# Kernel tuning notes

Hardware: AMD Instinct MI355X
Metric: run time of the kernel (lower is better)

## Reference

```python
import jax, jax.numpy as jnp
import numpy as np

INPUT_DIM = 768
HIDDEN = 64
NUM_CLASSES = 1


def _uniform(key, shape, bound):
    return jax.random.uniform(key, shape, jnp.float32, -bound, bound)


def setup_inputs() -> dict:
    key = jax.random.key(0)
    ks = jax.random.split(key, 16)
    B, T = 128, 512
    bound = 1.0 / np.sqrt(HIDDEN)  # PyTorch RNN init range
    inp = {
        "x": jax.random.normal(ks[0], (B, T, INPUT_DIM), jnp.float32),
        "fixation_num": 1,
        # layer 0: input_dim -> hidden
        "W_ih0": _uniform(ks[1], (HIDDEN, INPUT_DIM), bound),
        "W_hh0": _uniform(ks[2], (HIDDEN, HIDDEN), bound),
        "b_ih0": _uniform(ks[3], (HIDDEN,), bound),
        "b_hh0": _uniform(ks[4], (HIDDEN,), bound),
        # layer 1
        "W_ih1": _uniform(ks[5], (HIDDEN, HIDDEN), bound),
        "W_hh1": _uniform(ks[6], (HIDDEN, HIDDEN), bound),
        "b_ih1": _uniform(ks[7], (HIDDEN,), bound),
        "b_hh1": _uniform(ks[8], (HIDDEN,), bound),
        # layer 2
        "W_ih2": _uniform(ks[9], (HIDDEN, HIDDEN), bound),
        "W_hh2": _uniform(ks[10], (HIDDEN, HIDDEN), bound),
        "b_ih2": _uniform(ks[11], (HIDDEN,), bound),
        "b_hh2": _uniform(ks[12], (HIDDEN,), bound),
        # final linear head
        "fc_w": _uniform(ks[13], (NUM_CLASSES, HIDDEN), bound),
        "fc_b": _uniform(ks[14], (NUM_CLASSES,), bound),
    }
    return inp


def _rnn_layer(x, W_ih, W_hh, b_ih, b_hh):
    # x: [B, T, In] -> hidden sequence [B, T, H]; vanilla tanh RNN, h0 = 0
    pre = jnp.einsum("bti,hi->bth", x, W_ih) + b_ih + b_hh  # input projection for all t
    B = x.shape[0]
    h0 = jnp.zeros((B, W_hh.shape[0]), x.dtype)

    def step(h, p_t):  # p_t: [B, H]
        h = jnp.tanh(p_t + h @ W_hh.T)
        return h, h

    _, hs = jax.lax.scan(step, h0, jnp.swapaxes(pre, 0, 1))  # hs: [T, B, H]
    return jnp.swapaxes(hs, 0, 1)


def reference(x, fixation_num, W_ih0, W_hh0, b_ih0, b_hh0,
              W_ih1, W_hh1, b_ih1, b_hh1,
              W_ih2, W_hh2, b_ih2, b_hh2, fc_w, fc_b):
    # fixation_num is unused by the original forward
    h = _rnn_layer(x, W_ih0, W_hh0, b_ih0, b_hh0)
    h = _rnn_layer(h, W_ih1, W_hh1, b_ih1, b_hh1)
    h = _rnn_layer(h, W_ih2, W_hh2, b_ih2, b_hh2)
    last = h[:, -1, :]  # [B, H]
    return last @ fc_w.T + fc_b  # [B, num_classes]
```

## Files before the change

### kernel.cpp

```cpp
#include <hip/hip_runtime.h>


typedef __fp16 h2_t __attribute__((ext_vector_type(2)));
typedef __fp16 h8_t __attribute__((ext_vector_type(8)));
typedef float  f4_t __attribute__((ext_vector_type(4)));

union F4H { float4 f; h2_t h[4]; };
union H8U { h2_t h2[4]; h8_t h8; };

__device__ __forceinline__ float fdot2(h2_t a, h2_t b, float c) {
    return __builtin_amdgcn_fdot2(a, b, c, false);
}
__device__ __forceinline__ h2_t pack_h2(float x, float y) {
    return __builtin_amdgcn_cvt_pkrtz(x, y);
}
__device__ __forceinline__ float tanh_fast(float x) {
    float e = __expf(2.0f * x);
    return 1.0f - 2.0f * __builtin_amdgcn_rcpf(e + 1.0f);
}

__global__ __launch_bounds__(256) void gemm_pre0(
    const float* __restrict__ x,
    const float* __restrict__ Wih,
    const float* __restrict__ bih, const float* __restrict__ bhh,
    float* __restrict__ pre0)
{
    const int tid = threadIdx.x;
    const int wv  = tid >> 6;
    const int l   = tid & 63;
    const int m   = l & 15;
    const int q   = l >> 4;
    const int rowB = blockIdx.x * 128 + wv * 32;

    const float* ax0 = x + (size_t)(rowB + m) * 768 + q * 8;
    const float* ax1 = x + (size_t)(rowB + 16 + m) * 768 + q * 8;

    float4 ar[2][2];
    float4 br[4][2];

    ar[0][0] = *(const float4*)ax0;       ar[0][1] = *(const float4*)(ax0 + 4);
    ar[1][0] = *(const float4*)ax1;       ar[1][1] = *(const float4*)(ax1 + 4);
#pragma unroll
    for (int nt = 0; nt < 4; ++nt) {
        const float* p = Wih + (size_t)(nt * 16 + m) * 768 + q * 8;
        br[nt][0] = *(const float4*)p;    br[nt][1] = *(const float4*)(p + 4);
    }

    f4_t acc[2][4];
#pragma unroll
    for (int mt = 0; mt < 2; ++mt)
#pragma unroll
        for (int nt = 0; nt < 4; ++nt)
#pragma unroll
            for (int i = 0; i < 4; ++i) acc[mt][nt][i] = 0.0f;

#pragma unroll
    for (int it = 0; it < 24; ++it) {
        H8U fa[2], fb[4];
#pragma unroll
        for (int mt = 0; mt < 2; ++mt) {
            fa[mt].h2[0] = pack_h2(ar[mt][0].x, ar[mt][0].y);
            fa[mt].h2[1] = pack_h2(ar[mt][0].z, ar[mt][0].w);
            fa[mt].h2[2] = pack_h2(ar[mt][1].x, ar[mt][1].y);
            fa[mt].h2[3] = pack_h2(ar[mt][1].z, ar[mt][1].w);
        }
#pragma unroll
        for (int nt = 0; nt < 4; ++nt) {
            fb[nt].h2[0] = pack_h2(br[nt][0].x, br[nt][0].y);
            fb[nt].h2[1] = pack_h2(br[nt][0].z, br[nt][0].w);
            fb[nt].h2[2] = pack_h2(br[nt][1].x, br[nt][1].y);
            fb[nt].h2[3] = pack_h2(br[nt][1].z, br[nt][1].w);
        }
        if (it + 1 < 24) {
            const int ko = (it + 1) * 32;
            ar[0][0] = *(const float4*)(ax0 + ko);
            ar[0][1] = *(const float4*)(ax0 + ko + 4);
            ar[1][0] = *(const float4*)(ax1 + ko);
            ar[1][1] = *(const float4*)(ax1 + ko + 4);
#pragma unroll
            for (int nt = 0; nt < 4; ++nt) {
                const float* p = Wih + (size_t)(nt * 16 + m) * 768 + q * 8 + ko;
                br[nt][0] = *(const float4*)p;
                br[nt][1] = *(const float4*)(p + 4);
            }
        }
#pragma unroll
        for (int mt = 0; mt < 2; ++mt)
#pragma unroll
            for (int nt = 0; nt < 4; ++nt)
                acc[mt][nt] = __builtin_amdgcn_mfma_f32_16x16x32_f16(
                    fa[mt].h8, fb[nt].h8, acc[mt][nt], 0, 0, 0);
    }

    float bn[4];
#pragma unroll
    for (int nt = 0; nt < 4; ++nt) bn[nt] = bih[nt * 16 + m] + bhh[nt * 16 + m];
#pragma unroll
    for (int mt = 0; mt < 2; ++mt)
#pragma unroll
        for (int i = 0; i < 4; ++i) {
            int row = rowB + mt * 16 + q * 4 + i;
            float* pr = pre0 + (size_t)row * 64 + m;
#pragma unroll
            for (int nt = 0; nt < 4; ++nt)
                pr[nt * 16] = acc[mt][nt][i] + bn[nt];
        }
}

__device__ __forceinline__ float layer_epoch(
    const __fp16* __restrict__ in0,
    __fp16* __restrict__ self0, int par,
    const h2_t* wA2, const h2_t* wB2, float bias, int j)
{
    __fp16*       selfPar  = self0 + par * 512;
    const __fp16* selfPrev = self0 + (par ^ 1) * 512;

    F4H u0[8], u1[8];
#pragma unroll
    for (int qq = 0; qq < 8; ++qq) u0[qq].f = *(const float4*)(in0 + qq * 8);

    float hN = 0.0f;
#pragma unroll
    for (int s = 0; s < 8; ++s) {
        const F4H* uc = (s & 1) ? u1 : u0;
        F4H*       un = (s & 1) ? u0 : u1;

        const __fp16* rc = (s == 0) ? (selfPrev + 7 * 64) : (selfPar + (s - 1) * 64);
        F4H uh[8];
#pragma unroll
        for (int qq = 0; qq < 8; ++qq) uh[qq].f = *(const float4*)(rc + qq * 8);

        if (s < 7) {
#pragma unroll
            for (int qq = 0; qq < 8; ++qq)
                un[qq].f = *(const float4*)(in0 + (s + 1) * 64 + qq * 8);
        }

        float x0 = 0.f, x1 = 0.f, x2 = 0.f, x3 = 0.f;
#pragma unroll
        for (int qq = 0; qq < 8; ++qq) {
            x0 = fdot2(wA2[qq * 4 + 0], uc[qq].h[0], x0);
            x1 = fdot2(wA2[qq * 4 + 1], uc[qq].h[1], x1);
            x2 = fdot2(wA2[qq * 4 + 2], uc[qq].h[2], x2);
            x3 = fdot2(wA2[qq * 4 + 3], uc[qq].h[3], x3);
        }
        float xs = (x0 + x1) + (x2 + x3) + bias;

        float a0 = 0.f, a1 = 0.f, a2 = 0.f, a3 = 0.f;
#pragma unroll
        for (int qq = 0; qq < 8; ++qq) {
            a0 = fdot2(wB2[qq * 4 + 0], uh[qq].h[0], a0);
            a1 = fdot2(wB2[qq * 4 + 1], uh[qq].h[1], a1);
            a2 = fdot2(wB2[qq * 4 + 2], uh[qq].h[2], a2);
            a3 = fdot2(wB2[qq * 4 + 3], uh[qq].h[3], a3);
        }
        hN = tanh_fast((a0 + a1) + (a2 + a3) + xs);
        selfPar[s * 64 + j] = (__fp16)hN;
    }
    return hN;
}

__global__ __launch_bounds__(192, 1) void rnn_fused(
    const float* __restrict__ pre0,
    const float* __restrict__ Whh0,
    const float* __restrict__ Wih1, const float* __restrict__ Whh1,
    const float* __restrict__ bih1, const float* __restrict__ bhh1,
    const float* __restrict__ Wih2, const float* __restrict__ Whh2,
    const float* __restrict__ bih2, const float* __restrict__ bhh2,
    const float* __restrict__ fcw, const float* __restrict__ fcb,
    float* __restrict__ out)
{
    const int tid = threadIdx.x;
    const int g   = tid >> 6;
    const int j   = tid & 63;
    const int b   = blockIdx.x;

    __shared__ __align__(16) __fp16 hb[3][2][8][64];

    const float* WA = (g == 0) ? Whh0 : ((g == 1) ? Wih1 : Wih2);
    const float* WB = (g == 0) ? Whh0 : ((g == 1) ? Whh1 : Whh2);
    h2_t wA2[32], wB2[32];
#pragma unroll
    for (int i = 0; i < 32; ++i) {
        wA2[i] = pack_h2(WA[j * 64 + 2 * i], WA[j * 64 + 2 * i + 1]);
        wB2[i] = pack_h2(WB[j * 64 + 2 * i], WB[j * 64 + 2 * i + 1]);
    }
    const float bias = (g == 0) ? 0.0f
                     : ((g == 1) ? (bih1[j] + bhh1[j]) : (bih2[j] + bhh2[j]));

#pragma unroll
    for (int i = 0; i < 8; ++i) ((unsigned int*)hb)[tid + 192 * i] = 0u;

    const size_t pbase = (size_t)b * 32768;
    float pc[8], pn[8];
    if (g == 0) {
#pragma unroll
        for (int s = 0; s < 8; ++s) pc[s] = pre0[pbase + s * 64 + j];
    }
    __syncthreads();

    float hLast = 0.0f;

    for (int e = 0; e < 66; ++e) {
        if (g == 0) {
            if (e < 64) {
                if (e < 63) {
#pragma unroll
                    for (int s = 0; s < 8; ++s)
                        pn[s] = pre0[pbase + (size_t)(e + 1) * 512 + s * 64 + j];
                }
                const int par = e & 1;
#pragma unroll
                for (int s = 0; s < 8; ++s) {
                    const __fp16* rc = (s == 0) ? hb[0][par ^ 1][7] : hb[0][par][s - 1];
                    float a0 = 0.f, a1 = 0.f, a2 = 0.f, a3 = 0.f;
#pragma unroll
                    for (int qq = 0; qq < 8; ++qq) {
                        F4H u; u.f = *(const float4*)&rc[qq * 8];
                        a0 = fdot2(wA2[qq * 4 + 0], u.h[0], a0);
                        a1 = fdot2(wA2[qq * 4 + 1], u.h[1], a1);
                        a2 = fdot2(wA2[qq * 4 + 2], u.h[2], a2);
                        a3 = fdot2(wA2[qq * 4 + 3], u.h[3], a3);
                    }
                    float hN = tanh_fast((a0 + a1) + (a2 + a3) + pc[s]);
                    hb[0][par][s][j] = (__fp16)hN;
                }
#pragma unroll
                for (int s = 0; s < 8; ++s) pc[s] = pn[s];
            }
        } else if (g == 1) {
            if (e >= 1 && e < 65) {
                const int par = (e - 1) & 1;
                layer_epoch(&hb[0][par][0][0], &hb[1][0][0][0], par,
                            wA2, wB2, bias, j);
            }
        } else {
            if (e >= 2) {
                const int par = e & 1;
                float hN = layer_epoch(&hb[1][par][0][0], &hb[2][0][0][0], par,
                                       wA2, wB2, bias, j);
                if (e == 65) hLast = hN;
            }
        }
        __syncthreads();
    }

    if (g == 2) {
        float v = hLast * fcw[j];
#pragma unroll
        for (int m = 1; m < 64; m <<= 1) v += __shfl_xor(v, m, 64);
        if (j == 0) out[b] = v + fcb[0];
    }
}

extern "C" void kernel_launch(void* const* d_in, const int* in_sizes, int n_in,
                              void* d_out, int out_size, void* d_ws, size_t ws_size,
                              hipStream_t stream) {
    const float* x    = (const float*)d_in[0];
    const float* Wih0 = (const float*)d_in[2];
    const float* Whh0 = (const float*)d_in[3];
    const float* bih0 = (const float*)d_in[4];
    const float* bhh0 = (const float*)d_in[5];
    const float* Wih1 = (const float*)d_in[6];
    const float* Whh1 = (const float*)d_in[7];
    const float* bih1 = (const float*)d_in[8];
    const float* bhh1 = (const float*)d_in[9];
    const float* Wih2 = (const float*)d_in[10];
    const float* Whh2 = (const float*)d_in[11];
    const float* bih2 = (const float*)d_in[12];
    const float* bhh2 = (const float*)d_in[13];
    const float* fcw  = (const float*)d_in[14];
    const float* fcb  = (const float*)d_in[15];
    float* out  = (float*)d_out;
    float* pre0 = (float*)d_ws;

    gemm_pre0<<<512, 256, 0, stream>>>(x, Wih0, bih0, bhh0, pre0);
    rnn_fused<<<128, 192, 0, stream>>>(pre0, Whh0, Wih1, Whh1, bih1, bhh1,
                                       Wih2, Whh2, bih2, bhh2, fcw, fcb, out);
}
```

Before: 463.0 us.

## Batch layer 1/2 input projections per epoch with MFMA into shared memory

For layers 1 and 2, the input-to-hidden projection for all 8 timesteps of an epoch is now computed up front with 16x16x32 f16 MFMA instructions. The results go to a shared-memory buffer, replacing the per-timestep fdot2 chain. The serial recurrent loop then only does the hidden-to-hidden dot product plus a shared-memory read, which shortens the per-step critical path of the two slower wave groups. The cost is extra LDS traffic and an MFMA tile that reads 16 rows where only 8 are valid; the extra rows are discarded. Correctness also relies on in-wave ordering of LDS writes and reads without a barrier.

```diff
diff --git a/kernel.cpp b/kernel.cpp
--- a/kernel.cpp
+++ b/kernel.cpp
@@ -5,8 +5,9 @@
 typedef __fp16 h8_t __attribute__((ext_vector_type(8)));
 typedef float  f4_t __attribute__((ext_vector_type(4)));
 
-union F4H { float4 f; h2_t h[4]; };
-union H8U { h2_t h2[4]; h8_t h8; };
+union F4H  { float4 f; h2_t h[4]; };
+union F4H8 { float4 f; h8_t h8; h2_t h2[4]; };
+union H8U  { h2_t h2[4]; h8_t h8; };
 
 __device__ __forceinline__ float fdot2(h2_t a, h2_t b, float c) {
     return __builtin_amdgcn_fdot2(a, b, c, false);
@@ -110,41 +111,45 @@
 __device__ __forceinline__ float layer_epoch(
     const __fp16* __restrict__ in0,
     __fp16* __restrict__ self0, int par,
-    const h2_t* wA2, const h2_t* wB2, float bias, int j)
+    const h2_t* wB2, const h8_t* wX, float* __restrict__ xb,
+    float bias, int j)
 {
     __fp16*       selfPar  = self0 + par * 512;
     const __fp16* selfPrev = self0 + (par ^ 1) * 512;
-
-    F4H u0[8], u1[8];
-#pragma unroll
-    for (int qq = 0; qq < 8; ++qq) u0[qq].f = *(const float4*)(in0 + qq * 8);
+    const int mm = j & 15;
+    const int q4 = j >> 4;
+
+    F4H8 A0, A1;
+    const __fp16* arow = in0 + mm * 64 + q4 * 8;
+    A0.f = *(const float4*)arow;
+    A1.f = *(const float4*)(arow + 32);
+
+    f4_t xacc[4];
+#pragma unroll
+    for (int nt = 0; nt < 4; ++nt) {
+#pragma unroll
+        for (int i = 0; i < 4; ++i) xacc[nt][i] = 0.0f;
+        xacc[nt] = __builtin_amdgcn_mfma_f32_16x16x32_f16(
+            A0.h8, wX[nt * 2 + 0], xacc[nt], 0, 0, 0);
+        xacc[nt] = __builtin_amdgcn_mfma_f32_16x16x32_f16(
+            A1.h8, wX[nt * 2 + 1], xacc[nt], 0, 0, 0);
+    }
+    if (j < 32) {
+#pragma unroll
+        for (int nt = 0; nt < 4; ++nt)
+#pragma unroll
+            for (int i = 0; i < 4; ++i)
+                xb[(q4 * 4 + i) * 64 + nt * 16 + mm] = xacc[nt][i];
+    }
 
     float hN = 0.0f;
 #pragma unroll
     for (int s = 0; s < 8; ++s) {
-        const F4H* uc = (s & 1) ? u1 : u0;
-        F4H*       un = (s & 1) ? u0 : u1;
-
         const __fp16* rc = (s == 0) ? (selfPrev + 7 * 64) : (selfPar + (s - 1) * 64);
         F4H uh[8];
 #pragma unroll
         for (int qq = 0; qq < 8; ++qq) uh[qq].f = *(const float4*)(rc + qq * 8);
-
-        if (s < 7) {
-#pragma unroll
-            for (int qq = 0; qq < 8; ++qq)
-                un[qq].f = *(const float4*)(in0 + (s + 1) * 64 + qq * 8);
-        }
-
-        float x0 = 0.f, x1 = 0.f, x2 = 0.f, x3 = 0.f;
-#pragma unroll
-        for (int qq = 0; qq < 8; ++qq) {
-            x0 = fdot2(wA2[qq * 4 + 0], uc[qq].h[0], x0);
-            x1 = fdot2(wA2[qq * 4 + 1], uc[qq].h[1], x1);
-            x2 = fdot2(wA2[qq * 4 + 2], uc[qq].h[2], x2);
-            x3 = fdot2(wA2[qq * 4 + 3], uc[qq].h[3], x3);
-        }
-        float xs = (x0 + x1) + (x2 + x3) + bias;
+        float xs = xb[s * 64 + j];
 
         float a0 = 0.f, a1 = 0.f, a2 = 0.f, a3 = 0.f;
 #pragma unroll
@@ -154,7 +159,7 @@
             a2 = fdot2(wB2[qq * 4 + 2], uh[qq].h[2], a2);
             a3 = fdot2(wB2[qq * 4 + 3], uh[qq].h[3], a3);
         }
-        hN = tanh_fast((a0 + a1) + (a2 + a3) + xs);
+        hN = tanh_fast((a0 + a1) + (a2 + a3) + xs + bias);
         selfPar[s * 64 + j] = (__fp16)hN;
     }
     return hN;
@@ -176,15 +181,30 @@
     const int b   = blockIdx.x;
 
     __shared__ __align__(16) __fp16 hb[3][2][8][64];
-
-    const float* WA = (g == 0) ? Whh0 : ((g == 1) ? Wih1 : Wih2);
+    __shared__ __align__(16) float  xb2[2][8][64];
+
     const float* WB = (g == 0) ? Whh0 : ((g == 1) ? Whh1 : Whh2);
-    h2_t wA2[32], wB2[32];
-#pragma unroll
-    for (int i = 0; i < 32; ++i) {
-        wA2[i] = pack_h2(WA[j * 64 + 2 * i], WA[j * 64 + 2 * i + 1]);
+    h2_t wB2[32];
+#pragma unroll
+    for (int i = 0; i < 32; ++i)
         wB2[i] = pack_h2(WB[j * 64 + 2 * i], WB[j * 64 + 2 * i + 1]);
-    }
+
+    const float* WX = (g == 1) ? Wih1 : ((g == 2) ? Wih2 : Whh0);
+    const int mm = j & 15, q4 = j >> 4;
+    h8_t wX[8];
+#pragma unroll
+    for (int nt = 0; nt < 4; ++nt)
+#pragma unroll
+        for (int c = 0; c < 2; ++c) {
+            const float* p = WX + (nt * 16 + mm) * 64 + c * 32 + q4 * 8;
+            float4 r0 = *(const float4*)p;
+            float4 r1 = *(const float4*)(p + 4);
+            H8U u;
+            u.h2[0] = pack_h2(r0.x, r0.y); u.h2[1] = pack_h2(r0.z, r0.w);
+            u.h2[2] = pack_h2(r1.x, r1.y); u.h2[3] = pack_h2(r1.z, r1.w);
+            wX[nt * 2 + c] = u.h8;
+        }
+
     const float bias = (g == 0) ? 0.0f
                      : ((g == 1) ? (bih1[j] + bhh1[j]) : (bih2[j] + bhh2[j]));
 
@@ -217,10 +237,10 @@
 #pragma unroll
                     for (int qq = 0; qq < 8; ++qq) {
                         F4H u; u.f = *(const float4*)&rc[qq * 8];
-                        a0 = fdot2(wA2[qq * 4 + 0], u.h[0], a0);
-                        a1 = fdot2(wA2[qq * 4 + 1], u.h[1], a1);
-                        a2 = fdot2(wA2[qq * 4 + 2], u.h[2], a2);
-                        a3 = fdot2(wA2[qq * 4 + 3], u.h[3], a3);
+                        a0 = fdot2(wB2[qq * 4 + 0], u.h[0], a0);
+                        a1 = fdot2(wB2[qq * 4 + 1], u.h[1], a1);
+                        a2 = fdot2(wB2[qq * 4 + 2], u.h[2], a2);
+                        a3 = fdot2(wB2[qq * 4 + 3], u.h[3], a3);
                     }
                     float hN = tanh_fast((a0 + a1) + (a2 + a3) + pc[s]);
                     hb[0][par][s][j] = (__fp16)hN;
@@ -232,13 +252,13 @@
             if (e >= 1 && e < 65) {
                 const int par = (e - 1) & 1;
                 layer_epoch(&hb[0][par][0][0], &hb[1][0][0][0], par,
-                            wA2, wB2, bias, j);
+                            wB2, wX, &xb2[0][0][0], bias, j);
             }
         } else {
             if (e >= 2) {
                 const int par = e & 1;
                 float hN = layer_epoch(&hb[1][par][0][0], &hb[2][0][0][0], par,
-                                       wA2, wB2, bias, j);
+                                       wB2, wX, &xb2[1][0][0], bias, j);
                 if (e == 65) hLast = hN;
             }
         }
```

Measured after the change: 430.5 us. -7.0%, faster.
